# Kernel tuning notes

Measured on AMD Instinct MI355X. Metric: run time of the kernel, lower is better.

## Reference

```python
import jax, jax.numpy as jnp
import numpy as np

N_BLOCK = 3; EMBED = 256; N_HEAD = 8; HEAD = EMBED // N_HEAD
N_AGENT = 8; SEQ = 256; BATCH = 64; ACT_DIM = 32
DECAY_SCALE = 1.0
EPS = 1e-6


def _decay_matrix():
    # Per-head decay kappas as in Mava Sable, decay over timesteps (pos // n_agent), causal mask.
    gammas = (1.0 - jnp.exp(jnp.linspace(jnp.log(1.0 / 32.0), jnp.log(1.0 / 512.0), N_HEAD))) * DECAY_SCALE
    t = (jnp.arange(SEQ) // N_AGENT).astype(jnp.float32)
    diff = t[:, None] - t[None, :]
    causal = jnp.arange(SEQ)[:, None] >= jnp.arange(SEQ)[None, :]
    return jnp.where(causal[None], gammas[:, None, None] ** diff[None], 0.0)  # [H,S,S]


def rmsnorm(x, scale):
    return x * jax.lax.rsqrt(jnp.mean(x * x, -1, keepdims=True) + EPS) * scale


def groupnorm(x, scale, bias):
    # GroupNorm with n_head groups over the feature dim, per position.
    B, S, E = x.shape
    xg = x.reshape(B, S, N_HEAD, HEAD)
    mu = xg.mean(-1, keepdims=True)
    var = ((xg - mu) ** 2).mean(-1, keepdims=True)
    xn = ((xg - mu) * jax.lax.rsqrt(var + 1e-5)).reshape(B, S, E)
    return xn * scale + bias


def retention(q_in, k_in, v_in, wq, wk, wv, wg, wo, gns, gnb, decay):
    # Parallel multi-scale retention: (Q K^T * D) V, groupnorm, swish gate from query input.
    B, S, E = q_in.shape
    q = (q_in @ wq).reshape(B, S, N_HEAD, HEAD).transpose(0, 2, 1, 3)
    k = (k_in @ wk).reshape(B, S, N_HEAD, HEAD).transpose(0, 2, 1, 3) / jnp.sqrt(jnp.float32(HEAD))
    v = (v_in @ wv).reshape(B, S, N_HEAD, HEAD).transpose(0, 2, 1, 3)
    scores = jnp.einsum('bhnd,bhmd->bhnm', q, k) * decay[None]
    ret = jnp.einsum('bhnm,bhmd->bhnd', scores, v)
    ret = groupnorm(ret.transpose(0, 2, 1, 3).reshape(B, S, E), gns, gnb)
    return (jax.nn.swish(q_in @ wg) * ret) @ wo


def swiglu(x, wg, w1, w2):
    return (jax.nn.swish(x @ wg) * (x @ w1)) @ w2


def forward(action, obs_rep, w_enc, ln0, wq1, wk1, wv1, wg1, wo1, gns1, gnb1, ln1,
            wq2, wk2, wv2, wg2, wo2, gns2, gnb2, ln2, swg, sw1, sw2, ln3,
            hw1, hb1, hln, hw2, hb2):
    decay = _decay_matrix()
    x = rmsnorm(jax.nn.gelu(action @ w_enc), ln0)
    for b in range(N_BLOCK):
        r1 = retention(x, x, x, wq1[b], wk1[b], wv1[b], wg1[b], wo1[b], gns1[b], gnb1[b], decay)
        x = rmsnorm(x + r1, ln1[b])
        r2 = retention(obs_rep, x, x, wq2[b], wk2[b], wv2[b], wg2[b], wo2[b], gns2[b], gnb2[b], decay)
        x = rmsnorm(obs_rep + r2, ln2[b])
        x = rmsnorm(x + swiglu(x, swg[b], sw1[b], sw2[b]), ln3[b])
    h = rmsnorm(jax.nn.gelu(x @ hw1 + hb1), hln)
    return h @ hw2 + hb2


def setup_inputs() -> dict:
    key = jax.random.key(0)
    ks = jax.random.split(key, 24)
    E, A, NB = EMBED, ACT_DIM, N_BLOCK
    s = 0.02
    return {
        'action': jax.random.uniform(ks[0], (BATCH, SEQ, A), jnp.float32),
        'obs_rep': jax.random.normal(ks[1], (BATCH, SEQ, E), jnp.float32),
        'w_enc': jax.random.normal(ks[2], (A, E), jnp.float32) * s,
        'ln0': jnp.ones((E,), jnp.float32),
        'wq1': jax.random.normal(ks[3], (NB, E, E), jnp.float32) * s,
        'wk1': jax.random.normal(ks[4], (NB, E, E), jnp.float32) * s,
        'wv1': jax.random.normal(ks[5], (NB, E, E), jnp.float32) * s,
        'wg1': jax.random.normal(ks[6], (NB, E, E), jnp.float32) * s,
        'wo1': jax.random.normal(ks[7], (NB, E, E), jnp.float32) * s,
        'gns1': jnp.ones((NB, E), jnp.float32),
        'gnb1': jnp.zeros((NB, E), jnp.float32),
        'ln1': jnp.ones((NB, E), jnp.float32),
        'wq2': jax.random.normal(ks[8], (NB, E, E), jnp.float32) * s,
        'wk2': jax.random.normal(ks[9], (NB, E, E), jnp.float32) * s,
        'wv2': jax.random.normal(ks[10], (NB, E, E), jnp.float32) * s,
        'wg2': jax.random.normal(ks[11], (NB, E, E), jnp.float32) * s,
        'wo2': jax.random.normal(ks[12], (NB, E, E), jnp.float32) * s,
        'gns2': jnp.ones((NB, E), jnp.float32),
        'gnb2': jnp.zeros((NB, E), jnp.float32),
        'ln2': jnp.ones((NB, E), jnp.float32),
        'swg': jax.random.normal(ks[13], (NB, E, E), jnp.float32) * s,
        'sw1': jax.random.normal(ks[14], (NB, E, E), jnp.float32) * s,
        'sw2': jax.random.normal(ks[15], (NB, E, E), jnp.float32) * s,
        'ln3': jnp.ones((NB, E), jnp.float32),
        'hw1': jax.random.normal(ks[16], (E, E), jnp.float32) * s,
        'hb1': jnp.zeros((E,), jnp.float32),
        'hln': jnp.ones((E,), jnp.float32),
        'hw2': jax.random.normal(ks[17], (E, A), jnp.float32) * s,
        'hb2': jnp.zeros((A,), jnp.float32),
    }


def reference(action, obs_rep, w_enc, ln0, wq1, wk1, wv1, wg1, wo1, gns1, gnb1, ln1,
              wq2, wk2, wv2, wg2, wo2, gns2, gnb2, ln2, swg, sw1, sw2, ln3,
              hw1, hb1, hln, hw2, hb2):
    return forward(action, obs_rep, w_enc, ln0, wq1, wk1, wv1, wg1, wo1, gns1, gnb1, ln1,
                   wq2, wk2, wv2, wg2, wo2, gns2, gnb2, ln2, swg, sw1, sw2, ln3,
                   hw1, hb1, hln, hw2, hb2)
```

## Files before the change

kernel.cpp:

```cpp
#include <hip/hip_runtime.h>
#include <cstdint>
#include <cmath>

typedef __attribute__((ext_vector_type(8))) short short8;
typedef __attribute__((ext_vector_type(4))) float floatx4;

#define DEV static __device__ __forceinline__

DEV float bf2f(uint16_t u) {
    union { uint32_t i; float f; } v; v.i = ((uint32_t)u) << 16; return v.f;
}
DEV uint16_t f2bf(float f) {
    union { float f; uint32_t i; } v; v.f = f;
    uint32_t r = (v.i + 0x7FFFu + ((v.i >> 16) & 1u)) >> 16;
    return (uint16_t)r;
}
DEV float swishf(float x) { return x / (1.f + __expf(-x)); }
DEV float geluf(float x) {
    const float c = 0.7978845608028654f;
    float t = tanhf(c * (x + 0.044715f * x * x * x));
    return 0.5f * x * (1.f + t);
}

#define CHUNK_E 8192
#define MAT_E   65536
#define APAD    264


struct TArg { const float* src[15]; };

__global__ __launch_bounds__(256) void tpose_k(TArg ta, uint16_t* __restrict__ arena) {
    int z = blockIdx.z;
    const float* src; uint16_t* dst;
    if (z == 0) {
        if (blockIdx.y) return;
        src = ta.src[0]; dst = arena;
    } else if (z <= 39) {
        int q = z - 1; int ti = q / 3, s = q % 3;
        src = ta.src[1 + ti] + (size_t)s * 65536;
        dst = arena + CHUNK_E + (size_t)(ti * 3 + s) * MAT_E;
    } else {
        src = ta.src[14]; dst = arena + CHUNK_E + (size_t)39 * MAT_E;
    }
    int k0 = blockIdx.y << 5;
    int n0 = blockIdx.x << 6;
    __shared__ __align__(16) uint16_t tile[32][72];
    int t = threadIdx.x;
    {
        int r = t >> 3, c = (t & 7) << 3;
        const float* s0 = src + (size_t)(k0 + r) * 256 + n0 + c;
        float4 f0 = *(const float4*)s0;
        float4 f1 = *(const float4*)(s0 + 4);
        tile[r][c + 0] = f2bf(f0.x); tile[r][c + 1] = f2bf(f0.y);
        tile[r][c + 2] = f2bf(f0.z); tile[r][c + 3] = f2bf(f0.w);
        tile[r][c + 4] = f2bf(f1.x); tile[r][c + 5] = f2bf(f1.y);
        tile[r][c + 6] = f2bf(f1.z); tile[r][c + 7] = f2bf(f1.w);
    }
    __syncthreads();
    {
        int n = t >> 2, c = (t & 3) << 3;
        uint16_t tmp[8];
#pragma unroll
        for (int j = 0; j < 8; ++j) tmp[j] = tile[c + j][n];
        *(uint4*)&dst[(size_t)(k0 >> 5) * CHUNK_E + (size_t)(n0 + n) * 32 + c] = *(uint4*)tmp;
    }
}

struct SegArgs {
    const float* action; const float* obs;
    uint16_t *actb, *obsb, *xb, *bq, *bk, *bv, *bg, *brg;
    const float *ln0, *hb1, *hln, *hw2, *hb2;
    float* outp;
    float l2g[8];
};

enum { EP_NONE = 0, EP_GELU_RMS = 1, EP_RESID_RMS = 2 };
enum { EP2_NONE = 0, EP2_SWIGLU = 1 };

template<int EPI, int K, int LDA, bool OG, int LDO, bool RL>
DEV void gemm_u(int m0,
                const uint16_t* __restrict__ A,
                const uint16_t* __restrict__ Wt,
                uint16_t* __restrict__ Og,
                uint16_t* __restrict__ Ol,
                const float* __restrict__ bias,
                const uint16_t* __restrict__ Rg,
                const uint16_t* __restrict__ Rl,
                const float* __restrict__ lnw,
                float (&rowsum)[8][32])
{
    const int t = threadIdx.x;
    const int w = t >> 6, lane = t & 63, l16 = lane & 15, lg = lane >> 4;
    constexpr int NC = K / 32;

    floatx4 acc[2][2];
#pragma unroll
    for (int i = 0; i < 2; ++i)
#pragma unroll
        for (int j = 0; j < 2; ++j) acc[i][j] = (floatx4){0.f, 0.f, 0.f, 0.f};

#pragma unroll
    for (int kc = 0; kc < NC; ++kc) {
        short8 aF[2], bF[2];
#pragma unroll
        for (int rt = 0; rt < 2; ++rt) {
            int row = (rt << 4) + l16;
            if constexpr (LDA != 0)
                aF[rt] = *(const short8*)(A + (size_t)row * LDA + (kc << 5) + (lg << 3));
            else
                aF[rt] = *(const short8*)(A + (size_t)(m0 + row) * K + (kc << 5) + (lg << 3));
        }
#pragma unroll
        for (int ct = 0; ct < 2; ++ct)
            bF[ct] = *(const short8*)(Wt + (size_t)kc * CHUNK_E +
                                      (size_t)((w << 5) + (ct << 4) + l16) * 32 + (lg << 3));
#pragma unroll
        for (int rt = 0; rt < 2; ++rt)
#pragma unroll
            for (int ct = 0; ct < 2; ++ct)
                acc[rt][ct] = __builtin_amdgcn_mfma_f32_16x16x32_bf16(
                    aF[rt], bF[ct], acc[rt][ct], 0, 0, 0);
    }

    float v[2][2][4];
#pragma unroll
    for (int rt = 0; rt < 2; ++rt)
#pragma unroll
        for (int ct = 0; ct < 2; ++ct)
#pragma unroll
            for (int r = 0; r < 4; ++r) {
                int row = (rt << 4) + (lg << 2) + r;
                int col = (w << 5) + (ct << 4) + l16;
                float x = acc[rt][ct][r];
                if constexpr (EPI == EP_GELU_RMS) {
                    if (bias) x += bias[col];
                    x = geluf(x);
                }
                if constexpr (EPI == EP_RESID_RMS) {
                    if constexpr (RL) x += bf2f(Rl[(size_t)row * APAD + col]);
                    else              x += bf2f(Rg[(size_t)(m0 + row) * 256 + col]);
                }
                v[rt][ct][r] = x;
            }

    if constexpr (EPI == EP_GELU_RMS || EPI == EP_RESID_RMS) {
#pragma unroll
        for (int rt = 0; rt < 2; ++rt)
#pragma unroll
            for (int r = 0; r < 4; ++r) {
                float p = v[rt][0][r] * v[rt][0][r] + v[rt][1][r] * v[rt][1][r];
                p += __shfl_xor(p, 1, 64); p += __shfl_xor(p, 2, 64);
                p += __shfl_xor(p, 4, 64); p += __shfl_xor(p, 8, 64);
                int row = (rt << 4) + (lg << 2) + r;
                if (l16 == 0) rowsum[w][row] = p;
            }
        __syncthreads();
#pragma unroll
        for (int rt = 0; rt < 2; ++rt)
#pragma unroll
            for (int r = 0; r < 4; ++r) {
                int row = (rt << 4) + (lg << 2) + r;
                float tot = rowsum[0][row] + rowsum[1][row] + rowsum[2][row] + rowsum[3][row]
                          + rowsum[4][row] + rowsum[5][row] + rowsum[6][row] + rowsum[7][row];
                float rn = rsqrtf(tot * (1.f / 256.f) + 1e-6f);
#pragma unroll
                for (int ct = 0; ct < 2; ++ct) {
                    int col = (w << 5) + (ct << 4) + l16;
                    uint16_t bb = f2bf(v[rt][ct][r] * rn * lnw[col]);
                    if constexpr (OG)
                        Og[(size_t)(m0 + row) * 256 + col] = bb;
                    if constexpr (LDO != 0)
                        Ol[(size_t)row * LDO + col] = bb;
                }
            }
        __syncthreads();
    } else {
#pragma unroll
        for (int rt = 0; rt < 2; ++rt)
#pragma unroll
            for (int ct = 0; ct < 2; ++ct)
#pragma unroll
                for (int r = 0; r < 4; ++r) {
                    int row = (rt << 4) + (lg << 2) + r;
                    int col = (w << 5) + (ct << 4) + l16;
                    uint16_t bb = f2bf(v[rt][ct][r]);
                    if constexpr (OG)
                        Og[(size_t)(m0 + row) * 256 + col] = bb;
                    if constexpr (LDO != 0)
                        Ol[(size_t)row * LDO + col] = bb;
                }
    }
}

template<int EPI, int LDA>
DEV void gemm2_u(int m0, const uint16_t* __restrict__ A,
                 const uint16_t* __restrict__ W1, const uint16_t* __restrict__ W2,
                 uint16_t* __restrict__ O1, uint16_t* __restrict__ O2,
                 uint16_t* __restrict__ Ol)
{
    const int t = threadIdx.x;
    const int w = t >> 6, lane = t & 63, l16 = lane & 15, lg = lane >> 4;

    floatx4 a1[2][2], a2[2][2];
#pragma unroll
    for (int i = 0; i < 2; ++i)
#pragma unroll
        for (int j = 0; j < 2; ++j) {
            a1[i][j] = (floatx4){0.f, 0.f, 0.f, 0.f};
            a2[i][j] = (floatx4){0.f, 0.f, 0.f, 0.f};
        }

#pragma unroll
    for (int kc = 0; kc < 8; ++kc) {
        short8 aF[2], b1[2], b2[2];
#pragma unroll
        for (int rt = 0; rt < 2; ++rt) {
            int row = (rt << 4) + l16;
            if constexpr (LDA != 0)
                aF[rt] = *(const short8*)(A + (size_t)row * LDA + (kc << 5) + (lg << 3));
            else
                aF[rt] = *(const short8*)(A + (size_t)(m0 + row) * 256 + (kc << 5) + (lg << 3));
        }
        size_t woff = (size_t)kc * CHUNK_E + (size_t)((w << 5) + l16) * 32 + (lg << 3);
#pragma unroll
        for (int ct = 0; ct < 2; ++ct) {
            b1[ct] = *(const short8*)(W1 + woff + (size_t)(ct << 4) * 32);
            b2[ct] = *(const short8*)(W2 + woff + (size_t)(ct << 4) * 32);
        }
#pragma unroll
        for (int rt = 0; rt < 2; ++rt)
#pragma unroll
            for (int ct = 0; ct < 2; ++ct) {
                a1[rt][ct] = __builtin_amdgcn_mfma_f32_16x16x32_bf16(aF[rt], b1[ct], a1[rt][ct], 0, 0, 0);
                a2[rt][ct] = __builtin_amdgcn_mfma_f32_16x16x32_bf16(aF[rt], b2[ct], a2[rt][ct], 0, 0, 0);
            }
    }

#pragma unroll
    for (int rt = 0; rt < 2; ++rt)
#pragma unroll
        for (int ct = 0; ct < 2; ++ct)
#pragma unroll
            for (int r = 0; r < 4; ++r) {
                int row = (rt << 4) + (lg << 2) + r;
                int col = (w << 5) + (ct << 4) + l16;
                if constexpr (EPI == EP2_NONE) {
                    size_t idx = (size_t)(m0 + row) * 256 + col;
                    O1[idx] = f2bf(a1[rt][ct][r]);
                    O2[idx] = f2bf(a2[rt][ct][r]);
                } else {
                    Ol[(size_t)row * APAD + col] = f2bf(swishf(a1[rt][ct][r]) * a2[rt][ct][r]);
                }
            }
}

DEV int rowbase(int blk) { return (blk & 63) * 256 + (blk >> 6) * 32; }


__global__ __launch_bounds__(512, 4) void seg0_k(SegArgs sa, const uint16_t* __restrict__ wenc,
                                                 const uint16_t* __restrict__ wq,
                                                 const uint16_t* __restrict__ wk,
                                                 const uint16_t* __restrict__ wv,
                                                 const uint16_t* __restrict__ wg)
{
    __shared__ float rowsum[8][32];
    __shared__ __align__(16) uint16_t actS[32][40];
    __shared__ __align__(16) uint16_t T0[32][APAD];
    const int t = threadIdx.x;
    const int m0 = rowbase(blockIdx.x);
    if (t < 256) {
        int r = t >> 3, c = (t & 7) << 2;
        float4 f = *(const float4*)(sa.action + (size_t)(m0 + r) * 32 + c);
        uint16_t tmp[4] = { f2bf(f.x), f2bf(f.y), f2bf(f.z), f2bf(f.w) };
        *(uint2*)&actS[r][c] = *(uint2*)tmp;
    }
    {
        const float4* ob = (const float4*)sa.obs + (size_t)m0 * 64;
        uint2* od = (uint2*)sa.obsb + (size_t)m0 * 64;
#pragma unroll
        for (int j = 0; j < 4; ++j) {
            float4 f = ob[(j << 9) + t];
            uint16_t tmp[4] = { f2bf(f.x), f2bf(f.y), f2bf(f.z), f2bf(f.w) };
            od[(j << 9) + t] = *(uint2*)tmp;
        }
    }
    __syncthreads();
    gemm_u<EP_GELU_RMS, 32, 40, true, APAD, false>(m0, &actS[0][0], wenc,
        sa.xb, &T0[0][0], nullptr, nullptr, nullptr, sa.ln0, rowsum);
    gemm2_u<EP2_NONE, APAD>(m0, &T0[0][0], wq, wk, sa.bq, sa.bk, nullptr);
    gemm2_u<EP2_NONE, APAD>(m0, &T0[0][0], wv, wg, sa.bv, sa.bg, nullptr);
}

__global__ __launch_bounds__(512, 4) void attn_k(SegArgs sa, const float* __restrict__ gns,
                                                 const float* __restrict__ gnb)
{
    __shared__ __align__(16) uint16_t QS[256][40];
    __shared__ __align__(16) uint16_t Ks[256][40];
    __shared__ __align__(16) uint16_t Vt[32][264];
    const int b = blockIdx.x & 63, h = blockIdx.x >> 6;
    const float l2g = sa.l2g[h];
    const int t = threadIdx.x, w = t >> 6, lane = t & 63, l16 = lane & 15, lg = lane >> 4;
    const size_t base = ((size_t)b * 256) * 256 + (size_t)h * 32;
    const uint16_t *q = sa.bq, *kbuf = sa.bk, *vbuf = sa.bv, *g = sa.bg;
    uint16_t* out = sa.brg;

    if (t < 256) {
        const uint4* qr = (const uint4*)(q + base + (size_t)t * 256);
        *(uint4*)&QS[t][0] = qr[0]; *(uint4*)&QS[t][8] = qr[1];
        *(uint4*)&QS[t][16] = qr[2]; *(uint4*)&QS[t][24] = qr[3];
        const uint4* kr = (const uint4*)(kbuf + base + (size_t)t * 256);
        *(uint4*)&Ks[t][0] = kr[0]; *(uint4*)&Ks[t][8] = kr[1];
        *(uint4*)&Ks[t][16] = kr[2]; *(uint4*)&Ks[t][24] = kr[3];
    } else {
        int c = t - 256;
        union { uint4 v4[4]; uint16_t u[32]; } vv;
        const uint4* vr = (const uint4*)(vbuf + base + (size_t)c * 256);
        vv.v4[0] = vr[0]; vv.v4[1] = vr[1]; vv.v4[2] = vr[2]; vv.v4[3] = vr[3];
#pragma unroll
        for (int d = 0; d < 32; ++d) Vt[d][c] = vv.u[d];
    }
    __syncthreads();

    short8 qF[2];
#pragma unroll
    for (int rt = 0; rt < 2; ++rt)
        qF[rt] = *(const short8*)&QS[(w << 5) + (rt << 4) + l16][lg << 3];

    floatx4 racc[2][2];
#pragma unroll
    for (int i = 0; i < 2; ++i) { racc[i][0] = (floatx4){0,0,0,0}; racc[i][1] = (floatx4){0,0,0,0}; }

    const float invsq = 0.17677669529663687f;
    const int jtmax = w;
    for (int jt = 0; jt <= jtmax; ++jt) {
        const int j0 = jt << 5;
        floatx4 sacc[2][2];
#pragma unroll
        for (int i = 0; i < 2; ++i) { sacc[i][0] = (floatx4){0,0,0,0}; sacc[i][1] = (floatx4){0,0,0,0}; }
        short8 kF[2];
#pragma unroll
        for (int ct = 0; ct < 2; ++ct)
            kF[ct] = *(const short8*)&Ks[j0 + (ct << 4) + l16][lg << 3];
#pragma unroll
        for (int rt = 0; rt < 2; ++rt)
#pragma unroll
            for (int ct = 0; ct < 2; ++ct)
                sacc[rt][ct] = __builtin_amdgcn_mfma_f32_16x16x32_bf16(
                    qF[rt], kF[ct], sacc[rt][ct], 0, 0, 0);
#pragma unroll
        for (int rt = 0; rt < 2; ++rt)
#pragma unroll
            for (int ct = 0; ct < 2; ++ct)
#pragma unroll
                for (int r = 0; r < 4; ++r) {
                    int row = (rt << 4) + (lg << 2) + r;
                    int i = (w << 5) + row;
                    int j = j0 + (ct << 4) + l16;
                    float svv = 0.f;
                    if (i >= j)
                        svv = sacc[rt][ct][r] * invsq *
                              exp2f((float)((i >> 3) - (j >> 3)) * l2g);
                    QS[(w << 5) + row][(ct << 4) + l16] = f2bf(svv);
                }
        short8 vF[2];
#pragma unroll
        for (int ct = 0; ct < 2; ++ct)
            vF[ct] = *(const short8*)&Vt[(ct << 4) + l16][j0 + (lg << 3)];
#pragma unroll
        for (int rt = 0; rt < 2; ++rt) {
            short8 sF = *(const short8*)&QS[(w << 5) + (rt << 4) + l16][lg << 3];
#pragma unroll
            for (int ct = 0; ct < 2; ++ct)
                racc[rt][ct] = __builtin_amdgcn_mfma_f32_16x16x32_bf16(
                    sF, vF[ct], racc[rt][ct], 0, 0, 0);
        }
    }

#pragma unroll
    for (int rt = 0; rt < 2; ++rt)
#pragma unroll
        for (int r = 0; r < 4; ++r) {
            float v0 = racc[rt][0][r], v1 = racc[rt][1][r];
            float s1 = v0 + v1, s2 = v0 * v0 + v1 * v1;
            s1 += __shfl_xor(s1, 1, 64); s2 += __shfl_xor(s2, 1, 64);
            s1 += __shfl_xor(s1, 2, 64); s2 += __shfl_xor(s2, 2, 64);
            s1 += __shfl_xor(s1, 4, 64); s2 += __shfl_xor(s2, 4, 64);
            s1 += __shfl_xor(s1, 8, 64); s2 += __shfl_xor(s2, 8, 64);
            float mu = s1 * (1.f / 32.f);
            float var = s2 * (1.f / 32.f) - mu * mu;
            float rstd = rsqrtf(var + 1e-5f);
            int srow = (w << 5) + (rt << 4) + (lg << 2) + r;
            size_t obase = ((size_t)b * 256 + srow) * 256 + (size_t)h * 32;
#pragma unroll
            for (int ct = 0; ct < 2; ++ct) {
                int d = (ct << 4) + l16;
                float x = ct ? v1 : v0;
                float y = (x - mu) * rstd * gns[h * 32 + d] + gnb[h * 32 + d];
                float gv = swishf(bf2f(g[obase + d]));
                out[obase + d] = f2bf(y * gv);
            }
        }
}

__global__ __launch_bounds__(512, 4) void g1_k(SegArgs sa,
    const uint16_t* __restrict__ wo, const float* __restrict__ ln1,
    const uint16_t* __restrict__ wq, const uint16_t* __restrict__ wk,
    const uint16_t* __restrict__ wv, const uint16_t* __restrict__ wg)
{
    __shared__ float rowsum[8][32];
    __shared__ __align__(16) uint16_t T0[32][APAD];
    const int m0 = rowbase(blockIdx.x);
    gemm_u<EP_RESID_RMS, 256, 0, false, APAD, false>(m0, sa.brg, wo,
        nullptr, &T0[0][0], nullptr, sa.xb, nullptr, ln1, rowsum);
    gemm2_u<EP2_NONE, APAD>(m0, &T0[0][0], wk, wv, sa.bk, sa.bv, nullptr);
    gemm2_u<EP2_NONE, 0>(m0, sa.obsb, wq, wg, sa.bq, sa.bg, nullptr);
}

__global__ __launch_bounds__(512, 4) void g2_k(SegArgs sa,
    const uint16_t* __restrict__ wo, const float* __restrict__ ln2,
    const uint16_t* __restrict__ wswg, const uint16_t* __restrict__ wsw1,
    const uint16_t* __restrict__ wsw2, const float* __restrict__ ln3,
    const uint16_t* __restrict__ nwq, const uint16_t* __restrict__ nwk,
    const uint16_t* __restrict__ nwv, const uint16_t* __restrict__ nwg)
{
    __shared__ float rowsum[8][32];
    __shared__ __align__(16) uint16_t T0[32][APAD];
    __shared__ __align__(16) uint16_t T1[32][APAD];
    const int m0 = rowbase(blockIdx.x);
    gemm_u<EP_RESID_RMS, 256, 0, false, APAD, false>(m0, sa.brg, wo,
        nullptr, &T0[0][0], nullptr, sa.obsb, nullptr, ln2, rowsum);
    gemm2_u<EP2_SWIGLU, APAD>(m0, &T0[0][0], wswg, wsw1, nullptr, nullptr, &T1[0][0]);
    __syncthreads();
    gemm_u<EP_RESID_RMS, 256, APAD, true, APAD, true>(m0, &T1[0][0], wsw2,
        sa.xb, &T0[0][0], nullptr, nullptr, &T0[0][0], ln3, rowsum);
    if (nwq) {
        gemm2_u<EP2_NONE, APAD>(m0, &T0[0][0], nwq, nwk, sa.bq, sa.bk, nullptr);
        gemm2_u<EP2_NONE, APAD>(m0, &T0[0][0], nwv, nwg, sa.bv, sa.bg, nullptr);
    }
}

__global__ __launch_bounds__(512, 4) void head_k(SegArgs sa, const uint16_t* __restrict__ hw1t)
{
    __shared__ float rowsum[8][32];
    __shared__ float w2s[8192];
    __shared__ __align__(16) uint16_t T0[32][APAD];
    const int t = threadIdx.x;
    const int m0 = rowbase(blockIdx.x);
#pragma unroll
    for (int j = 0; j < 16; ++j) w2s[(j << 9) + t] = sa.hw2[(j << 9) + t];
    gemm_u<EP_GELU_RMS, 256, 0, false, APAD, false>(m0, sa.xb, hw1t,
        nullptr, &T0[0][0], sa.hb1, nullptr, nullptr, sa.hln, rowsum);
    {
        int n = t & 31, rs = t >> 5;
#pragma unroll
        for (int rr = 0; rr < 2; ++rr) {
            int lrow = (rr << 4) + rs;
            float a0 = sa.hb2[n];
#pragma unroll 8
            for (int kk = 0; kk < 256; ++kk)
                a0 += bf2f(T0[lrow][kk]) * w2s[kk * 32 + n];
            sa.outp[(size_t)(m0 + lrow) * 32 + n] = a0;
        }
    }
}

extern "C" void kernel_launch(void* const* d_in, const int* in_sizes, int n_in,
                              void* d_out, int out_size, void* d_ws, size_t ws_size,
                              hipStream_t stream)
{
    const float* action = (const float*)d_in[0];
    const float* obs    = (const float*)d_in[1];
    const float* w_enc  = (const float*)d_in[2];
    const float* ln0    = (const float*)d_in[3];
    const float* wq1 = (const float*)d_in[4];
    const float* wk1 = (const float*)d_in[5];
    const float* wv1 = (const float*)d_in[6];
    const float* wg1 = (const float*)d_in[7];
    const float* wo1 = (const float*)d_in[8];
    const float* gns1 = (const float*)d_in[9];
    const float* gnb1 = (const float*)d_in[10];
    const float* ln1  = (const float*)d_in[11];
    const float* wq2 = (const float*)d_in[12];
    const float* wk2 = (const float*)d_in[13];
    const float* wv2 = (const float*)d_in[14];
    const float* wg2 = (const float*)d_in[15];
    const float* wo2 = (const float*)d_in[16];
    const float* gns2 = (const float*)d_in[17];
    const float* gnb2 = (const float*)d_in[18];
    const float* ln2  = (const float*)d_in[19];
    const float* swgp = (const float*)d_in[20];
    const float* sw1p = (const float*)d_in[21];
    const float* sw2p = (const float*)d_in[22];
    const float* ln3  = (const float*)d_in[23];
    const float* hw1  = (const float*)d_in[24];
    const float* hb1  = (const float*)d_in[25];
    const float* hln  = (const float*)d_in[26];
    const float* hw2  = (const float*)d_in[27];
    const float* hb2  = (const float*)d_in[28];

    char* ws = (char*)d_ws;
    uint16_t* wt   = (uint16_t*)(ws + 0);
    uint16_t* actb = (uint16_t*)(ws + 6291456);
    uint16_t* obsb = (uint16_t*)(ws + 7340032);
    uint16_t* xb   = (uint16_t*)(ws + 15728640);
    uint16_t* bq   = (uint16_t*)(ws + 24117248);
    uint16_t* bk   = (uint16_t*)(ws + 32505856);
    uint16_t* bv   = (uint16_t*)(ws + 40894464);
    uint16_t* bg   = (uint16_t*)(ws + 49283072);
    uint16_t* brg  = (uint16_t*)(ws + 57671680);

    uint16_t* wtenc = wt;
    uint16_t* hw1t  = wt + CHUNK_E + (size_t)39 * MAT_E;
    auto WTp = [&](int ti, int s) { return wt + CHUNK_E + (size_t)(ti * 3 + s) * MAT_E; };

    TArg ta;
    ta.src[0] = w_enc;
    ta.src[1] = wq1;  ta.src[2] = wk1;  ta.src[3] = wv1;  ta.src[4] = wg1;  ta.src[5] = wo1;
    ta.src[6] = wq2;  ta.src[7] = wk2;  ta.src[8] = wv2;  ta.src[9] = wg2;  ta.src[10] = wo2;
    ta.src[11] = swgp; ta.src[12] = sw1p; ta.src[13] = sw2p; ta.src[14] = hw1;
    tpose_k<<<dim3(4, 8, 41), 256, 0, stream>>>(ta, wt);

    SegArgs sa;
    sa.action = action; sa.obs = obs;
    sa.actb = actb; sa.obsb = obsb; sa.xb = xb;
    sa.bq = bq; sa.bk = bk; sa.bv = bv; sa.bg = bg; sa.brg = brg;
    sa.ln0 = ln0; sa.hb1 = hb1; sa.hln = hln; sa.hw2 = hw2; sa.hb2 = hb2;
    sa.outp = (float*)d_out;
    {
        const double a = log(1.0 / 32.0), bb = log(1.0 / 512.0);
        for (int hh = 0; hh < 8; ++hh) {
            double lg = a + (bb - a) * hh / 7.0;
            double gam = 1.0 - exp(lg);
            sa.l2g[hh] = (float)(log(gam) / log(2.0));
        }
    }

    dim3 GB(512), TB(512);
    seg0_k<<<GB, TB, 0, stream>>>(sa, wtenc, WTp(0, 0), WTp(1, 0), WTp(2, 0), WTp(3, 0));
    for (int b3 = 0; b3 < 3; ++b3) {
        attn_k<<<GB, TB, 0, stream>>>(sa, gns1 + b3 * 256, gnb1 + b3 * 256);
        g1_k<<<GB, TB, 0, stream>>>(sa, WTp(4, b3), ln1 + b3 * 256,
                                    WTp(5, b3), WTp(6, b3), WTp(7, b3), WTp(8, b3));
        attn_k<<<GB, TB, 0, stream>>>(sa, gns2 + b3 * 256, gnb2 + b3 * 256);
        g2_k<<<GB, TB, 0, stream>>>(sa, WTp(9, b3), ln2 + b3 * 256,
                                    WTp(10, b3), WTp(11, b3), WTp(12, b3), ln3 + b3 * 256,
                                    b3 < 2 ? WTp(0, b3 + 1) : nullptr,
                                    b3 < 2 ? WTp(1, b3 + 1) : nullptr,
                                    b3 < 2 ? WTp(2, b3 + 1) : nullptr,
                                    b3 < 2 ? WTp(3, b3 + 1) : nullptr);
    }
    head_k<<<GB, TB, 0, stream>>>(sa, hw1t);
}
```

Measured before the change: 555.1 us.

## Use 64-row GEMM tiles, packed bf16 stores, and balanced causal attention strips

Doubles the GEMM row tile from 32 to 64 rows per block, halving the grid for the GEMM kernels so each weight fragment is reused across twice as many rows. Weight columns are permuted during transpose so each lane owns two adjacent output columns, which lets epilogues write packed 32-bit bf16 pairs and load bias, residual and norm weights as pairs. Global A inputs are staged into LDS first. The attention kernel gives each warp a short and a long causal strip (i and 15-i) to even out triangular work. The trade-off is more LDS and registers per block, which may lower occupancy.

```diff
diff --git a/kernel.cpp b/kernel.cpp
--- a/kernel.cpp
+++ b/kernel.cpp
@@ -14,6 +14,9 @@
     union { float f; uint32_t i; } v; v.f = f;
     uint32_t r = (v.i + 0x7FFFu + ((v.i >> 16) & 1u)) >> 16;
     return (uint16_t)r;
+}
+DEV uint32_t pk2(float lo, float hi) {
+    return (uint32_t)f2bf(lo) | ((uint32_t)f2bf(hi) << 16);
 }
 DEV float swishf(float x) { return x / (1.f + __expf(-x)); }
 DEV float geluf(float x) {
@@ -59,10 +62,12 @@
     __syncthreads();
     {
         int n = t >> 2, c = (t & 3) << 3;
+        int gc = n0 + n;
+        int np = (gc & ~31) | ((gc & 1) << 4) | ((gc & 31) >> 1);
         uint16_t tmp[8];
 #pragma unroll
         for (int j = 0; j < 8; ++j) tmp[j] = tile[c + j][n];
-        *(uint4*)&dst[(size_t)(k0 >> 5) * CHUNK_E + (size_t)(n0 + n) * 32 + c] = *(uint4*)tmp;
+        *(uint4*)&dst[(size_t)(k0 >> 5) * CHUNK_E + (size_t)np * 32 + c] = *(uint4*)tmp;
     }
 }
 
@@ -76,6 +81,17 @@
 
 enum { EP_NONE = 0, EP_GELU_RMS = 1, EP_RESID_RMS = 2 };
 enum { EP2_NONE = 0, EP2_SWIGLU = 1 };
+
+DEV void stage64(const uint16_t* __restrict__ g, int m0, uint16_t* __restrict__ lds) {
+    const int t = threadIdx.x;
+#pragma unroll
+    for (int j = 0; j < 4; ++j) {
+        int c = t + (j << 9);
+        int r = c >> 5, cc = (c & 31) << 3;
+        short8 v = *(const short8*)(g + (size_t)(m0 + r) * 256 + cc);
+        *(short8*)(lds + (size_t)r * APAD + cc) = v;
+    }
+}
 
 template<int EPI, int K, int LDA, bool OG, int LDO, bool RL>
 DEV void gemm_u(int m0,
@@ -87,23 +103,24 @@
                 const uint16_t* __restrict__ Rg,
                 const uint16_t* __restrict__ Rl,
                 const float* __restrict__ lnw,
-                float (&rowsum)[8][32])
+                float (&rowsum)[8][64])
 {
     const int t = threadIdx.x;
     const int w = t >> 6, lane = t & 63, l16 = lane & 15, lg = lane >> 4;
+    const int cb2 = (w << 5) + (l16 << 1);
     constexpr int NC = K / 32;
 
-    floatx4 acc[2][2];
-#pragma unroll
-    for (int i = 0; i < 2; ++i)
+    floatx4 acc[4][2];
+#pragma unroll
+    for (int i = 0; i < 4; ++i)
 #pragma unroll
         for (int j = 0; j < 2; ++j) acc[i][j] = (floatx4){0.f, 0.f, 0.f, 0.f};
 
 #pragma unroll
     for (int kc = 0; kc < NC; ++kc) {
-        short8 aF[2], bF[2];
-#pragma unroll
-        for (int rt = 0; rt < 2; ++rt) {
+        short8 aF[4], bF[2];
+#pragma unroll
+        for (int rt = 0; rt < 4; ++rt) {
             int row = (rt << 4) + l16;
             if constexpr (LDA != 0)
                 aF[rt] = *(const short8*)(A + (size_t)row * LDA + (kc << 5) + (lg << 3));
@@ -115,80 +132,73 @@
             bF[ct] = *(const short8*)(Wt + (size_t)kc * CHUNK_E +
                                       (size_t)((w << 5) + (ct << 4) + l16) * 32 + (lg << 3));
 #pragma unroll
-        for (int rt = 0; rt < 2; ++rt)
+        for (int rt = 0; rt < 4; ++rt)
 #pragma unroll
             for (int ct = 0; ct < 2; ++ct)
                 acc[rt][ct] = __builtin_amdgcn_mfma_f32_16x16x32_bf16(
                     aF[rt], bF[ct], acc[rt][ct], 0, 0, 0);
     }
 
-    float v[2][2][4];
-#pragma unroll
-    for (int rt = 0; rt < 2; ++rt)
-#pragma unroll
-        for (int ct = 0; ct < 2; ++ct)
+    float v0[4][4], v1[4][4];
+#pragma unroll
+    for (int rt = 0; rt < 4; ++rt)
+#pragma unroll
+        for (int r = 0; r < 4; ++r) {
+            int row = (rt << 4) + (lg << 2) + r;
+            float x0 = acc[rt][0][r], x1 = acc[rt][1][r];
+            if constexpr (EPI == EP_GELU_RMS) {
+                if (bias) { float2 bb = *(const float2*)(bias + cb2); x0 += bb.x; x1 += bb.y; }
+                x0 = geluf(x0); x1 = geluf(x1);
+            }
+            if constexpr (EPI == EP_RESID_RMS) {
+                uint32_t rr;
+                if constexpr (RL) rr = *(const uint32_t*)(Rl + (size_t)row * APAD + cb2);
+                else              rr = *(const uint32_t*)(Rg + (size_t)(m0 + row) * 256 + cb2);
+                x0 += bf2f((uint16_t)rr); x1 += bf2f((uint16_t)(rr >> 16));
+            }
+            v0[rt][r] = x0; v1[rt][r] = x1;
+        }
+
+    if constexpr (EPI == EP_GELU_RMS || EPI == EP_RESID_RMS) {
+#pragma unroll
+        for (int rt = 0; rt < 4; ++rt)
 #pragma unroll
             for (int r = 0; r < 4; ++r) {
-                int row = (rt << 4) + (lg << 2) + r;
-                int col = (w << 5) + (ct << 4) + l16;
-                float x = acc[rt][ct][r];
-                if constexpr (EPI == EP_GELU_RMS) {
-                    if (bias) x += bias[col];
-                    x = geluf(x);
-                }
-                if constexpr (EPI == EP_RESID_RMS) {
-                    if constexpr (RL) x += bf2f(Rl[(size_t)row * APAD + col]);
-                    else              x += bf2f(Rg[(size_t)(m0 + row) * 256 + col]);
-                }
-                v[rt][ct][r] = x;
-            }
-
-    if constexpr (EPI == EP_GELU_RMS || EPI == EP_RESID_RMS) {
-#pragma unroll
-        for (int rt = 0; rt < 2; ++rt)
-#pragma unroll
-            for (int r = 0; r < 4; ++r) {
-                float p = v[rt][0][r] * v[rt][0][r] + v[rt][1][r] * v[rt][1][r];
+                float p = v0[rt][r] * v0[rt][r] + v1[rt][r] * v1[rt][r];
                 p += __shfl_xor(p, 1, 64); p += __shfl_xor(p, 2, 64);
                 p += __shfl_xor(p, 4, 64); p += __shfl_xor(p, 8, 64);
                 int row = (rt << 4) + (lg << 2) + r;
                 if (l16 == 0) rowsum[w][row] = p;
             }
         __syncthreads();
-#pragma unroll
-        for (int rt = 0; rt < 2; ++rt)
+        float2 lw = *(const float2*)(lnw + cb2);
+#pragma unroll
+        for (int rt = 0; rt < 4; ++rt)
 #pragma unroll
             for (int r = 0; r < 4; ++r) {
                 int row = (rt << 4) + (lg << 2) + r;
                 float tot = rowsum[0][row] + rowsum[1][row] + rowsum[2][row] + rowsum[3][row]
                           + rowsum[4][row] + rowsum[5][row] + rowsum[6][row] + rowsum[7][row];
                 float rn = rsqrtf(tot * (1.f / 256.f) + 1e-6f);
-#pragma unroll
-                for (int ct = 0; ct < 2; ++ct) {
-                    int col = (w << 5) + (ct << 4) + l16;
-                    uint16_t bb = f2bf(v[rt][ct][r] * rn * lnw[col]);
-                    if constexpr (OG)
-                        Og[(size_t)(m0 + row) * 256 + col] = bb;
-                    if constexpr (LDO != 0)
-                        Ol[(size_t)row * LDO + col] = bb;
-                }
+                uint32_t pkv = pk2(v0[rt][r] * rn * lw.x, v1[rt][r] * rn * lw.y);
+                if constexpr (OG)
+                    *(uint32_t*)(Og + (size_t)(m0 + row) * 256 + cb2) = pkv;
+                if constexpr (LDO != 0)
+                    *(uint32_t*)(Ol + (size_t)row * LDO + cb2) = pkv;
             }
         __syncthreads();
     } else {
 #pragma unroll
-        for (int rt = 0; rt < 2; ++rt)
-#pragma unroll
-            for (int ct = 0; ct < 2; ++ct)
-#pragma unroll
-                for (int r = 0; r < 4; ++r) {
-                    int row = (rt << 4) + (lg << 2) + r;
-                    int col = (w << 5) + (ct << 4) + l16;
-                    uint16_t bb = f2bf(v[rt][ct][r]);
-                    if constexpr (OG)
-                        Og[(size_t)(m0 + row) * 256 + col] = bb;
-                    if constexpr (LDO != 0)
-                        Ol[(size_t)row * LDO + col] = bb;
-                }
+        for (int rt = 0; rt < 4; ++rt)
+#pragma unroll
+            for (int r = 0; r < 4; ++r) {
+                int row = (rt << 4) + (lg << 2) + r;
+                uint32_t pkv = pk2(v0[rt][r], v1[rt][r]);
+                if constexpr (OG)
+                    *(uint32_t*)(Og + (size_t)(m0 + row) * 256 + cb2) = pkv;
+                if constexpr (LDO != 0)
+                    *(uint32_t*)(Ol + (size_t)row * LDO + cb2) = pkv;
+            }
     }
 }
 
@@ -200,10 +210,11 @@
 {
     const int t = threadIdx.x;
     const int w = t >> 6, lane = t & 63, l16 = lane & 15, lg = lane >> 4;
-
-    floatx4 a1[2][2], a2[2][2];
-#pragma unroll
-    for (int i = 0; i < 2; ++i)
+    const int cb2 = (w << 5) + (l16 << 1);
+
+    floatx4 a1[4][2], a2[4][2];
+#pragma unroll
+    for (int i = 0; i < 4; ++i)
 #pragma unroll
         for (int j = 0; j < 2; ++j) {
             a1[i][j] = (floatx4){0.f, 0.f, 0.f, 0.f};
@@ -212,15 +223,10 @@
 
 #pragma unroll
     for (int kc = 0; kc < 8; ++kc) {
-        short8 aF[2], b1[2], b2[2];
-#pragma unroll
-        for (int rt = 0; rt < 2; ++rt) {
-            int row = (rt << 4) + l16;
-            if constexpr (LDA != 0)
-                aF[rt] = *(const short8*)(A + (size_t)row * LDA + (kc << 5) + (lg << 3));
-            else
-                aF[rt] = *(const short8*)(A + (size_t)(m0 + row) * 256 + (kc << 5) + (lg << 3));
-        }
+        short8 aF[4], b1[2], b2[2];
+#pragma unroll
+        for (int rt = 0; rt < 4; ++rt)
+            aF[rt] = *(const short8*)(A + (size_t)((rt << 4) + l16) * LDA + (kc << 5) + (lg << 3));
         size_t woff = (size_t)kc * CHUNK_E + (size_t)((w << 5) + l16) * 32 + (lg << 3);
 #pragma unroll
         for (int ct = 0; ct < 2; ++ct) {
@@ -228,7 +234,7 @@
             b2[ct] = *(const short8*)(W2 + woff + (size_t)(ct << 4) * 32);
         }
 #pragma unroll
-        for (int rt = 0; rt < 2; ++rt)
+        for (int rt = 0; rt < 4; ++rt)
 #pragma unroll
             for (int ct = 0; ct < 2; ++ct) {
                 a1[rt][ct] = __builtin_amdgcn_mfma_f32_16x16x32_bf16(aF[rt], b1[ct], a1[rt][ct], 0, 0, 0);
@@ -237,24 +243,23 @@
     }
 
 #pragma unroll
-    for (int rt = 0; rt < 2; ++rt)
-#pragma unroll
-        for (int ct = 0; ct < 2; ++ct)
-#pragma unroll
-            for (int r = 0; r < 4; ++r) {
-                int row = (rt << 4) + (lg << 2) + r;
-                int col = (w << 5) + (ct << 4) + l16;
-                if constexpr (EPI == EP2_NONE) {
-                    size_t idx = (size_t)(m0 + row) * 256 + col;
-                    O1[idx] = f2bf(a1[rt][ct][r]);
-                    O2[idx] = f2bf(a2[rt][ct][r]);
-                } else {
-                    Ol[(size_t)row * APAD + col] = f2bf(swishf(a1[rt][ct][r]) * a2[rt][ct][r]);
-                }
-            }
-}
-
-DEV int rowbase(int blk) { return (blk & 63) * 256 + (blk >> 6) * 32; }
+    for (int rt = 0; rt < 4; ++rt)
+#pragma unroll
+        for (int r = 0; r < 4; ++r) {
+            int row = (rt << 4) + (lg << 2) + r;
+            if constexpr (EPI == EP2_NONE) {
+                size_t idx = (size_t)(m0 + row) * 256 + cb2;
+                *(uint32_t*)(O1 + idx) = pk2(a1[rt][0][r], a1[rt][1][r]);
+                *(uint32_t*)(O2 + idx) = pk2(a2[rt][0][r], a2[rt][1][r]);
+            } else {
+                *(uint32_t*)(Ol + (size_t)row * APAD + cb2) =
+                    pk2(swishf(a1[rt][0][r]) * a2[rt][0][r],
+                        swishf(a1[rt][1][r]) * a2[rt][1][r]);
+            }
+        }
+}
+
+DEV int rowbase64(int blk) { return (blk & 63) * 256 + (blk >> 6) * 64; }
 
 
 __global__ __launch_bounds__(512, 4) void seg0_k(SegArgs sa, const uint16_t* __restrict__ wenc,
@@ -263,12 +268,12 @@
                                                  const uint16_t* __restrict__ wv,
                                                  const uint16_t* __restrict__ wg)
 {
-    __shared__ float rowsum[8][32];
-    __shared__ __align__(16) uint16_t actS[32][40];
-    __shared__ __align__(16) uint16_t T0[32][APAD];
+    __shared__ float rowsum[8][64];
+    __shared__ __align__(16) uint16_t actS[64][40];
+    __shared__ __align__(16) uint16_t T0[64][APAD];
     const int t = threadIdx.x;
-    const int m0 = rowbase(blockIdx.x);
-    if (t < 256) {
+    const int m0 = rowbase64(blockIdx.x);
+    {
         int r = t >> 3, c = (t & 7) << 2;
         float4 f = *(const float4*)(sa.action + (size_t)(m0 + r) * 32 + c);
         uint16_t tmp[4] = { f2bf(f.x), f2bf(f.y), f2bf(f.z), f2bf(f.w) };
@@ -278,7 +283,7 @@
         const float4* ob = (const float4*)sa.obs + (size_t)m0 * 64;
         uint2* od = (uint2*)sa.obsb + (size_t)m0 * 64;
 #pragma unroll
-        for (int j = 0; j < 4; ++j) {
+        for (int j = 0; j < 8; ++j) {
             float4 f = ob[(j << 9) + t];
             uint16_t tmp[4] = { f2bf(f.x), f2bf(f.y), f2bf(f.z), f2bf(f.w) };
             od[(j << 9) + t] = *(uint2*)tmp;
@@ -321,66 +326,61 @@
     }
     __syncthreads();
 
-    short8 qF[2];
-#pragma unroll
-    for (int rt = 0; rt < 2; ++rt)
-        qF[rt] = *(const short8*)&QS[(w << 5) + (rt << 4) + l16][lg << 3];
-
-    floatx4 racc[2][2];
-#pragma unroll
-    for (int i = 0; i < 2; ++i) { racc[i][0] = (floatx4){0,0,0,0}; racc[i][1] = (floatx4){0,0,0,0}; }
+    const int iA = w, iB = 15 - w;
+    short8 qFA = *(const short8*)&QS[(iA << 4) + l16][lg << 3];
+    short8 qFB = *(const short8*)&QS[(iB << 4) + l16][lg << 3];
 
     const float invsq = 0.17677669529663687f;
-    const int jtmax = w;
-    for (int jt = 0; jt <= jtmax; ++jt) {
-        const int j0 = jt << 5;
-        floatx4 sacc[2][2];
-#pragma unroll
-        for (int i = 0; i < 2; ++i) { sacc[i][0] = (floatx4){0,0,0,0}; sacc[i][1] = (floatx4){0,0,0,0}; }
-        short8 kF[2];
-#pragma unroll
-        for (int ct = 0; ct < 2; ++ct)
-            kF[ct] = *(const short8*)&Ks[j0 + (ct << 4) + l16][lg << 3];
-#pragma unroll
-        for (int rt = 0; rt < 2; ++rt)
+
+    floatx4 raccA[2], raccB[2];
+    raccA[0] = (floatx4){0,0,0,0}; raccA[1] = (floatx4){0,0,0,0};
+    raccB[0] = (floatx4){0,0,0,0}; raccB[1] = (floatx4){0,0,0,0};
+
+    auto do_strip = [&](int si, short8 qF, floatx4 (&racc)[2]) {
+        const int jtmax = ((si << 4) + 15) >> 5;
+        for (int jt = 0; jt <= jtmax; ++jt) {
+            const int j0 = jt << 5;
+            floatx4 sacc[2];
+            sacc[0] = (floatx4){0,0,0,0}; sacc[1] = (floatx4){0,0,0,0};
+            short8 kF[2];
 #pragma unroll
             for (int ct = 0; ct < 2; ++ct)
-                sacc[rt][ct] = __builtin_amdgcn_mfma_f32_16x16x32_bf16(
-                    qF[rt], kF[ct], sacc[rt][ct], 0, 0, 0);
-#pragma unroll
-        for (int rt = 0; rt < 2; ++rt)
+                kF[ct] = *(const short8*)&Ks[j0 + (ct << 4) + l16][lg << 3];
 #pragma unroll
             for (int ct = 0; ct < 2; ++ct)
+                sacc[ct] = __builtin_amdgcn_mfma_f32_16x16x32_bf16(
+                    qF, kF[ct], sacc[ct], 0, 0, 0);
+#pragma unroll
+            for (int ct = 0; ct < 2; ++ct)
 #pragma unroll
                 for (int r = 0; r < 4; ++r) {
-                    int row = (rt << 4) + (lg << 2) + r;
-                    int i = (w << 5) + row;
+                    int row16 = (lg << 2) + r;
+                    int i = (si << 4) + row16;
                     int j = j0 + (ct << 4) + l16;
                     float svv = 0.f;
                     if (i >= j)
-                        svv = sacc[rt][ct][r] * invsq *
+                        svv = sacc[ct][r] * invsq *
                               exp2f((float)((i >> 3) - (j >> 3)) * l2g);
-                    QS[(w << 5) + row][(ct << 4) + l16] = f2bf(svv);
+                    QS[(si << 4) + row16][(ct << 4) + l16] = f2bf(svv);
                 }
-        short8 vF[2];
-#pragma unroll
-        for (int ct = 0; ct < 2; ++ct)
-            vF[ct] = *(const short8*)&Vt[(ct << 4) + l16][j0 + (lg << 3)];
-#pragma unroll
-        for (int rt = 0; rt < 2; ++rt) {
-            short8 sF = *(const short8*)&QS[(w << 5) + (rt << 4) + l16][lg << 3];
+            short8 vF[2];
 #pragma unroll
             for (int ct = 0; ct < 2; ++ct)
-                racc[rt][ct] = __builtin_amdgcn_mfma_f32_16x16x32_bf16(
-                    sF, vF[ct], racc[rt][ct], 0, 0, 0);
-        }
-    }
-
-#pragma unroll
-    for (int rt = 0; rt < 2; ++rt)
+                vF[ct] = *(const short8*)&Vt[(ct << 4) + l16][j0 + (lg << 3)];
+            short8 sF = *(const short8*)&QS[(si << 4) + l16][lg << 3];
+#pragma unroll
+            for (int ct = 0; ct < 2; ++ct)
+                racc[ct] = __builtin_amdgcn_mfma_f32_16x16x32_bf16(
+                    sF, vF[ct], racc[ct], 0, 0, 0);
+        }
+    };
+    do_strip(iA, qFA, raccA);
+    do_strip(iB, qFB, raccB);
+
+    auto epi = [&](int si, floatx4 (&racc)[2]) {
 #pragma unroll
         for (int r = 0; r < 4; ++r) {
-            float v0 = racc[rt][0][r], v1 = racc[rt][1][r];
+            float v0 = racc[0][r], v1 = racc[1][r];
             float s1 = v0 + v1, s2 = v0 * v0 + v1 * v1;
             s1 += __shfl_xor(s1, 1, 64); s2 += __shfl_xor(s2, 1, 64);
             s1 += __shfl_xor(s1, 2, 64); s2 += __shfl_xor(s2, 2, 64);
@@ -389,7 +389,7 @@
             float mu = s1 * (1.f / 32.f);
             float var = s2 * (1.f / 32.f) - mu * mu;
             float rstd = rsqrtf(var + 1e-5f);
-            int srow = (w << 5) + (rt << 4) + (lg << 2) + r;
+            int srow = (si << 4) + (lg << 2) + r;
             size_t obase = ((size_t)b * 256 + srow) * 256 + (size_t)h * 32;
 #pragma unroll
             for (int ct = 0; ct < 2; ++ct) {
@@ -400,6 +400,9 @@
                 out[obase + d] = f2bf(y * gv);
             }
         }
+    };
+    epi(iA, raccA);
+    epi(iB, raccB);
 }
 
 __global__ __launch_bounds__(512, 4) void g1_k(SegArgs sa,
@@ -407,13 +410,18 @@
     const uint16_t* __restrict__ wq, const uint16_t* __restrict__ wk,
     const uint16_t* __restrict__ wv, const uint16_t* __restrict__ wg)
 {
-    __shared__ float rowsum[8][32];
-    __shared__ __align__(16) uint16_t T0[32][APAD];
-    const int m0 = rowbase(blockIdx.x);
-    gemm_u<EP_RESID_RMS, 256, 0, false, APAD, false>(m0, sa.brg, wo,
+    __shared__ float rowsum[8][64];
+    __shared__ __align__(16) uint16_t T0[64][APAD];
+    __shared__ __align__(16) uint16_t T1[64][APAD];
+    const int m0 = rowbase64(blockIdx.x);
+    stage64(sa.brg, m0, &T1[0][0]);
+    __syncthreads();
+    gemm_u<EP_RESID_RMS, 256, APAD, false, APAD, false>(m0, &T1[0][0], wo,
         nullptr, &T0[0][0], nullptr, sa.xb, nullptr, ln1, rowsum);
+    stage64(sa.obsb, m0, &T1[0][0]);
     gemm2_u<EP2_NONE, APAD>(m0, &T0[0][0], wk, wv, sa.bk, sa.bv, nullptr);
-    gemm2_u<EP2_NONE, 0>(m0, sa.obsb, wq, wg, sa.bq, sa.bg, nullptr);
+    __syncthreads();
+    gemm2_u<EP2_NONE, APAD>(m0, &T1[0][0], wq, wg, sa.bq, sa.bg, nullptr);
 }
 
 __global__ __launch_bounds__(512, 4) void g2_k(SegArgs sa,
@@ -423,11 +431,13 @@
     const uint16_t* __restrict__ nwq, const uint16_t* __restrict__ nwk,
     const uint16_t* __restrict__ nwv, const uint16_t* __restrict__ nwg)
 {
-    __shared__ float rowsum[8][32];
-    __shared__ __align__(16) uint16_t T0[32][APAD];
-    __shared__ __align__(16) uint16_t T1[32][APAD];
-    const int m0 = rowbase(blockIdx.x);
-    gemm_u<EP_RESID_RMS, 256, 0, false, APAD, false>(m0, sa.brg, wo,
+    __shared__ float rowsum[8][64];
+    __shared__ __align__(16) uint16_t T0[64][APAD];
+    __shared__ __align__(16) uint16_t T1[64][APAD];
+    const int m0 = rowbase64(blockIdx.x);
+    stage64(sa.brg, m0, &T1[0][0]);
+    __syncthreads();
+    gemm_u<EP_RESID_RMS, 256, APAD, false, APAD, false>(m0, &T1[0][0], wo,
         nullptr, &T0[0][0], nullptr, sa.obsb, nullptr, ln2, rowsum);
     gemm2_u<EP2_SWIGLU, APAD>(m0, &T0[0][0], wswg, wsw1, nullptr, nullptr, &T1[0][0]);
     __syncthreads();
@@ -441,11 +451,11 @@
 
 __global__ __launch_bounds__(512, 4) void head_k(SegArgs sa, const uint16_t* __restrict__ hw1t)
 {
-    __shared__ float rowsum[8][32];
+    __shared__ float rowsum[8][64];
     __shared__ float w2s[8192];
-    __shared__ __align__(16) uint16_t T0[32][APAD];
+    __shared__ __align__(16) uint16_t T0[64][APAD];
     const int t = threadIdx.x;
-    const int m0 = rowbase(blockIdx.x);
+    const int m0 = rowbase64(blockIdx.x);
 #pragma unroll
     for (int j = 0; j < 16; ++j) w2s[(j << 9) + t] = sa.hw2[(j << 9) + t];
     gemm_u<EP_GELU_RMS, 256, 0, false, APAD, false>(m0, sa.xb, hw1t,
@@ -453,7 +463,7 @@
     {
         int n = t & 31, rs = t >> 5;
 #pragma unroll
-        for (int rr = 0; rr < 2; ++rr) {
+        for (int rr = 0; rr < 4; ++rr) {
             int lrow = (rr << 4) + rs;
             float a0 = sa.hb2[n];
 #pragma unroll 8
@@ -535,19 +545,19 @@
         }
     }
 
-    dim3 GB(512), TB(512);
-    seg0_k<<<GB, TB, 0, stream>>>(sa, wtenc, WTp(0, 0), WTp(1, 0), WTp(2, 0), WTp(3, 0));
+    dim3 GBg(256), GBa(512), TB(512);
+    seg0_k<<<GBg, TB, 0, stream>>>(sa, wtenc, WTp(0, 0), WTp(1, 0), WTp(2, 0), WTp(3, 0));
     for (int b3 = 0; b3 < 3; ++b3) {
-        attn_k<<<GB, TB, 0, stream>>>(sa, gns1 + b3 * 256, gnb1 + b3 * 256);
-        g1_k<<<GB, TB, 0, stream>>>(sa, WTp(4, b3), ln1 + b3 * 256,
-                                    WTp(5, b3), WTp(6, b3), WTp(7, b3), WTp(8, b3));
-        attn_k<<<GB, TB, 0, stream>>>(sa, gns2 + b3 * 256, gnb2 + b3 * 256);
-        g2_k<<<GB, TB, 0, stream>>>(sa, WTp(9, b3), ln2 + b3 * 256,
-                                    WTp(10, b3), WTp(11, b3), WTp(12, b3), ln3 + b3 * 256,
-                                    b3 < 2 ? WTp(0, b3 + 1) : nullptr,
-                                    b3 < 2 ? WTp(1, b3 + 1) : nullptr,
-                                    b3 < 2 ? WTp(2, b3 + 1) : nullptr,
-                                    b3 < 2 ? WTp(3, b3 + 1) : nullptr);
-    }
-    head_k<<<GB, TB, 0, stream>>>(sa, hw1t);
-}
+        attn_k<<<GBa, TB, 0, stream>>>(sa, gns1 + b3 * 256, gnb1 + b3 * 256);
+        g1_k<<<GBg, TB, 0, stream>>>(sa, WTp(4, b3), ln1 + b3 * 256,
+                                     WTp(5, b3), WTp(6, b3), WTp(7, b3), WTp(8, b3));
+        attn_k<<<GBa, TB, 0, stream>>>(sa, gns2 + b3 * 256, gnb2 + b3 * 256);
+        g2_k<<<GBg, TB, 0, stream>>>(sa, WTp(9, b3), ln2 + b3 * 256,
+                                     WTp(10, b3), WTp(11, b3), WTp(12, b3), ln3 + b3 * 256,
+                                     b3 < 2 ? WTp(0, b3 + 1) : nullptr,
+                                     b3 < 2 ? WTp(1, b3 + 1) : nullptr,
+                                     b3 < 2 ? WTp(2, b3 + 1) : nullptr,
+                                     b3 < 2 ? WTp(3, b3 + 1) : nullptr);
+    }
+    head_k<<<GBg, TB, 0, stream>>>(sa, hw1t);
+}
```

After: 631.4 us. 1.14x slower.
